# Kernel tuning notes

Measured on AMD Instinct MI355X. Metric: run time of the kernel, lower is better.

The kernel has to match this reference:

```python
import jax, jax.numpy as jnp
import numpy as np

N = 3072
SIGMA = 1.0
NORM_FACTOR = 90.4756
TWOPI = 2.0 * np.pi
NORM_CONST = NORM_FACTOR / TWOPI
A = 1.0 / (SIGMA * 2.0 ** 0.5)
SQRT_PI = np.pi ** 0.5


def setup_inputs() -> dict:
    key = jax.random.key(0)
    ks = jax.random.split(key, 6)
    q = jax.random.normal(ks[0], (N,), dtype=jnp.float32)
    r = jax.random.uniform(ks[1], (N, 3), dtype=jnp.float32) * 30.0  # 30A box
    cell = jnp.zeros((1, 3, 3), dtype=jnp.float32)  # det<1e-6 -> realspace path
    batch = jnp.zeros((N,), dtype=jnp.int32)
    u = jax.random.normal(ks[2], (N, 3), dtype=jnp.float32)
    kappa = jax.random.uniform(ks[3], (N,), dtype=jnp.float32)
    alpha = jax.random.uniform(ks[4], (N,), dtype=jnp.float32)
    return {"q": q, "r": r, "cell": cell, "batch": batch, "u": u, "kappa": kappa, "alpha": alpha}


def _ewald_realspace(q, r, u, kappa, alpha):
    # q:[n], r:[n,3], u:[n,3], kappa:[n], alpha:[n]; single batch, n_q=1 path
    n = q.shape[0]
    eye = jnp.eye(n, dtype=r.dtype)
    off = 1.0 - eye  # mask_off
    r_ij = r[None, :, :] - r[:, None, :]            # [n,n,3], r_j - r_i
    d2 = jnp.sum(r_ij * r_ij, axis=-1)
    rnorm = jnp.sqrt(d2 + eye)                      # diag padded with 1 for grad safety
    rinv = off / rnorm                              # 0 on diagonal
    rinv2 = rinv * rinv
    rinv3 = rinv2 * rinv
    erf = jax.scipy.special.erf(rnorm * A) * off    # 0 on diagonal
    gauss = jnp.exp(-(A * rnorm) ** 2) * off

    # charge-charge
    f_qq = erf * rinv * NORM_CONST
    e_phi = jnp.einsum('i,ij->j', q, f_qq)
    pot = 0.5 * jnp.dot(e_phi, q)

    # dipole kernels
    s1 = erf * rinv3 - (2.0 * A / SQRT_PI) * gauss * rinv2
    s2 = 3.0 * erf * rinv3 - (6.0 * A / SQRT_PI) * gauss * rinv2 - (4.0 * A ** 3 / SQRT_PI) * gauss

    # charge-dipole: f_qu[i,j,c] = s1[i,j]*r_ij[i,j,c]*NORM_CONST (contracted on the fly)
    ur = jnp.einsum('ic,ijc->ij', u, r_ij)          # u_i . r_ij
    e_phi_u = NORM_CONST * jnp.einsum('ij,ij->j', s1, ur)
    e_phi = e_phi + e_phi_u
    pot = pot + jnp.dot(e_phi_u, q)

    # dipole-dipole: f_uu = NORM_CONST*(s2 * rhat rhat^T - s1 * I), contracted without [n,n,3,3]
    rhat = r_ij * rinv[..., None]
    ai = jnp.einsum('ic,ijc->ij', u, rhat)          # u_i . rhat_ij
    bj = jnp.einsum('jc,ijc->ij', u, rhat)          # u_j . rhat_ij
    uu = u @ u.T
    pot = pot - 0.5 * NORM_CONST * (jnp.sum(s2 * ai * bj) - jnp.sum(s1 * uu))

    # induced charges (remove_self_interaction=True: no self terms)
    q_induced = -kappa * e_phi
    pot = pot + 0.5 * jnp.dot(e_phi, q_induced)

    # electric field (alpha is not None -> computed)
    e_field = NORM_CONST * jnp.einsum('i,ij,ijc->jc', q, s1, r_ij)
    E_u = NORM_CONST * (jnp.einsum('ij,ijd->jd', s2 * ai, rhat) - s1.T @ u)
    e_field = e_field + E_u

    # induced dipoles (alpha scalar per node)
    u_induced = e_field * alpha[:, None]
    pot = pot - 0.5 * jnp.sum(e_field * u_induced)

    return pot.reshape(1), q_induced, u_induced


def reference(q, r, cell, batch, u, kappa, alpha):
    # cell is zeros (det < 1e-6) and batch is all-zeros -> single-system realspace branch
    return _ewald_realspace(q, r, u, kappa, alpha)
```

## Files before the change

### kernel.cpp

```cpp
#include <hip/hip_runtime.h>
#include <hip/hip_bf16.h>

#define NATOMS 3072
#define CHUNKS 16
#define WPB 4
#define IPW (NATOMS / (CHUNKS * WPB))

static_assert(IPW * CHUNKS * WPB == NATOMS, "partition must cover all atoms");

constexpr float NCf = (float)(90.4756 / (2.0 * 3.14159265358979323846));
constexpr float Af = 0.70710678118654752f;
constexpr float Cf = 0.79788456080286536f;

__global__ __launch_bounds__(256)
void ewald_pack(const float* __restrict__ q, const float* __restrict__ r,
                const float* __restrict__ u, float4* __restrict__ P,
                float4* __restrict__ U) {
  const int i = blockIdx.x * blockDim.x + threadIdx.x;
  if (i < NATOMS) {
    P[i] = make_float4(r[3 * i + 0], r[3 * i + 1], r[3 * i + 2], q[i]);
    U[i] = make_float4(u[3 * i + 0], u[3 * i + 1], u[3 * i + 2], 0.0f);
  }
}

__global__ __launch_bounds__(256)
void ewald_main(const float4* __restrict__ P, const float4* __restrict__ U,
                float* __restrict__ part) {
  const int lane = threadIdx.x & 63;
  const int w = threadIdx.x >> 6;
  const int j = blockIdx.x * 64 + lane;
  const float4 pj = P[j];

  float acc[8] = {0.f, 0.f, 0.f, 0.f, 0.f, 0.f, 0.f, 0.f};

  const int i0 = (blockIdx.y * WPB + w) * IPW;
#pragma unroll 4
  for (int t = 0; t < IPW; ++t) {
    const int i = i0 + t;
    const float4 pi = P[i];
    const float4 ui = U[i];
    const float dx = pj.x - pi.x;
    const float dy = pj.y - pi.y;
    const float dz = pj.z - pi.z;
    float d2 = dx * dx + dy * dy + dz * dz;
    const bool diag = (i == j);
    if (diag) d2 = 1.0f;
    const float off = diag ? 0.0f : 1.0f;

    const float rinv = __builtin_amdgcn_rsqf(d2);
    const float rinv2 = rinv * rinv;
    const float rinv3 = rinv2 * rinv;
    const float rnorm = d2 * rinv;
    const float x = Af * rnorm;
    const float g0 = __expf(-0.5f * d2);
    const float tt = __builtin_amdgcn_rcpf(fmaf(0.3275911f, x, 1.0f));
    const float poly =
        tt * (0.254829592f +
              tt * (-0.284496736f +
                    tt * (1.421413741f +
                          tt * (-1.453152027f + tt * 1.061405429f))));
    const float erfv = (1.0f - poly * g0) * off;
    const float cg = Cf * (g0 * off);
    const float s1 = erfv * rinv3 - cg * rinv2;
    const float s2 = 3.0f * s1 - cg;

    acc[0] += pi.w * (erfv * rinv);
    const float ur = ui.x * dx + ui.y * dy + ui.z * dz;
    acc[1] += s1 * ur;
    const float qs1 = pi.w * s1;
    acc[2] += qs1 * dx;
    acc[3] += qs1 * dy;
    acc[4] += qs1 * dz;
    const float t2 = s2 * (ur * rinv) * rinv;
    acc[5] += t2 * dx - s1 * ui.x;
    acc[6] += t2 * dy - s1 * ui.y;
    acc[7] += t2 * dz - s1 * ui.z;
  }

  __shared__ float red[(WPB - 1) * 64 * 8];
  if (w > 0) {
    float* dst = &red[((w - 1) * 64 + lane) * 8];
#pragma unroll
    for (int k = 0; k < 8; ++k) dst[k] = acc[k];
  }
  __syncthreads();
  if (w == 0) {
#pragma unroll
    for (int ww = 0; ww < WPB - 1; ++ww) {
      const float* src = &red[(ww * 64 + lane) * 8];
#pragma unroll
      for (int k = 0; k < 8; ++k) acc[k] += src[k];
    }
    float4* dst = (float4*)&part[((size_t)blockIdx.y * NATOMS + j) * 8];
    dst[0] = make_float4(acc[0], acc[1], acc[2], acc[3]);
    dst[1] = make_float4(acc[4], acc[5], acc[6], acc[7]);
  }
}

__global__ __launch_bounds__(256)
void ewald_finalize(const float* __restrict__ part, const float* __restrict__ q,
                    const float* __restrict__ u, const float* __restrict__ kappa,
                    const float* __restrict__ alpha, float* __restrict__ out) {
  const int j = blockIdx.x * blockDim.x + threadIdx.x;

  float s[8] = {0.f, 0.f, 0.f, 0.f, 0.f, 0.f, 0.f, 0.f};
#pragma unroll
  for (int c = 0; c < CHUNKS; ++c) {
    const float4* src = (const float4*)&part[((size_t)c * NATOMS + j) * 8];
    const float4 a = src[0];
    const float4 b = src[1];
    s[0] += a.x; s[1] += a.y; s[2] += a.z; s[3] += a.w;
    s[4] += b.x; s[5] += b.y; s[6] += b.z; s[7] += b.w;
  }

  const float e_phi = NCf * (s[0] + s[1]);
  const float Eux = NCf * s[5];
  const float Euy = NCf * s[6];
  const float Euz = NCf * s[7];
  const float efx = NCf * s[2] + Eux;
  const float efy = NCf * s[3] + Euy;
  const float efz = NCf * s[4] + Euz;

  const float qj = q[j];
  const float kj = kappa[j];
  const float aj = alpha[j];
  const float ujx = u[3 * j + 0];
  const float ujy = u[3 * j + 1];
  const float ujz = u[3 * j + 2];

  out[1 + j] = -kj * e_phi;
  out[1 + NATOMS + 3 * j + 0] = aj * efx;
  out[1 + NATOMS + 3 * j + 1] = aj * efy;
  out[1 + NATOMS + 3 * j + 2] = aj * efz;

  float potj = 0.5f * NCf * s[0] * qj
             + NCf * s[1] * qj
             - 0.5f * (ujx * Eux + ujy * Euy + ujz * Euz)
             - 0.5f * kj * e_phi * e_phi
             - 0.5f * aj * (efx * efx + efy * efy + efz * efz);

#pragma unroll
  for (int m = 32; m >= 1; m >>= 1) potj += __shfl_xor(potj, m, 64);
  __shared__ float lred[4];
  const int lane = threadIdx.x & 63;
  const int wid = threadIdx.x >> 6;
  if (lane == 0) lred[wid] = potj;
  __syncthreads();
  if (threadIdx.x == 0) {
    atomicAdd(out, lred[0] + lred[1] + lred[2] + lred[3]);
  }
}

extern "C" void kernel_launch(void* const* d_in, const int* in_sizes, int n_in,
                              void* d_out, int out_size, void* d_ws,
                              size_t ws_size, hipStream_t stream) {
  const float* q = (const float*)d_in[0];
  const float* r = (const float*)d_in[1];
  const float* u = (const float*)d_in[4];
  const float* kappa = (const float*)d_in[5];
  const float* alpha = (const float*)d_in[6];
  float* out = (float*)d_out;

  float4* P = (float4*)d_ws;
  float4* U = P + NATOMS;
  float* part = (float*)(U + NATOMS);

  hipMemsetAsync(out, 0, sizeof(float), stream);
  ewald_pack<<<dim3((NATOMS + 255) / 256), 256, 0, stream>>>(q, r, u, P, U);
  ewald_main<<<dim3(NATOMS / 64, CHUNKS), 256, 0, stream>>>(P, U, part);
  ewald_finalize<<<dim3(NATOMS / 256), 256, 0, stream>>>(part, q, u, kappa,
                                                         alpha, out);
}
```

Before: 93.73 us.

## Fuse pack into main kernel with LDS staging and drop memset launch

Removes the separate pack kernel and the memset: each block of the main kernel loads its i-chunk of positions, charges and dipoles straight from the raw inputs into shared memory, and block (0,0) zeroes the potential output. CHUNKS doubles to 32, which doubles the grid and the partial buffer that finalize reads. The aim is to cut launch overhead and global-load latency in the inner loop, at the cost of more partial-sum traffic and an extra barrier.

```diff
diff --git a/kernel.cpp b/kernel.cpp
--- a/kernel.cpp
+++ b/kernel.cpp
@@ -2,46 +2,51 @@
 #include <hip/hip_bf16.h>
 
 #define NATOMS 3072
-#define CHUNKS 16
+#define CHUNKS 32
 #define WPB 4
-#define IPW (NATOMS / (CHUNKS * WPB))
+#define IPB (NATOMS / CHUNKS)
+#define IPW (IPB / WPB)
 
-static_assert(IPW * CHUNKS * WPB == NATOMS, "partition must cover all atoms");
+static_assert(IPB * CHUNKS == NATOMS, "i-partition must cover all atoms");
+static_assert(IPW * WPB == IPB, "wave split must cover block chunk");
 
 constexpr float NCf = (float)(90.4756 / (2.0 * 3.14159265358979323846));
 constexpr float Af = 0.70710678118654752f;
 constexpr float Cf = 0.79788456080286536f;
 
 __global__ __launch_bounds__(256)
-void ewald_pack(const float* __restrict__ q, const float* __restrict__ r,
-                const float* __restrict__ u, float4* __restrict__ P,
-                float4* __restrict__ U) {
-  const int i = blockIdx.x * blockDim.x + threadIdx.x;
-  if (i < NATOMS) {
-    P[i] = make_float4(r[3 * i + 0], r[3 * i + 1], r[3 * i + 2], q[i]);
-    U[i] = make_float4(u[3 * i + 0], u[3 * i + 1], u[3 * i + 2], 0.0f);
-  }
-}
-
-__global__ __launch_bounds__(256)
-void ewald_main(const float4* __restrict__ P, const float4* __restrict__ U,
-                float* __restrict__ part) {
+void ewald_main(const float* __restrict__ q, const float* __restrict__ r,
+                const float* __restrict__ u, float* __restrict__ part,
+                float* __restrict__ out) {
   const int lane = threadIdx.x & 63;
   const int w = threadIdx.x >> 6;
   const int j = blockIdx.x * 64 + lane;
-  const float4 pj = P[j];
+
+  if (blockIdx.x == 0 && blockIdx.y == 0 && threadIdx.x == 0) out[0] = 0.0f;
+
+  __shared__ float4 sPU[2 * IPB];
+  const int i0 = blockIdx.y * IPB;
+  for (int t = threadIdx.x; t < IPB; t += 256) {
+    const int i = i0 + t;
+    sPU[2 * t + 0] = make_float4(r[3 * i + 0], r[3 * i + 1], r[3 * i + 2], q[i]);
+    sPU[2 * t + 1] = make_float4(u[3 * i + 0], u[3 * i + 1], u[3 * i + 2], 0.0f);
+  }
+  const float pjx = r[3 * j + 0];
+  const float pjy = r[3 * j + 1];
+  const float pjz = r[3 * j + 2];
+  __syncthreads();
 
   float acc[8] = {0.f, 0.f, 0.f, 0.f, 0.f, 0.f, 0.f, 0.f};
 
-  const int i0 = (blockIdx.y * WPB + w) * IPW;
-#pragma unroll 4
-  for (int t = 0; t < IPW; ++t) {
+  const int t0 = w * IPW;
+#pragma unroll 6
+  for (int t = t0; t < t0 + IPW; ++t) {
+    const float4 pi = sPU[2 * t + 0];
+    const float4 ui = sPU[2 * t + 1];
     const int i = i0 + t;
-    const float4 pi = P[i];
-    const float4 ui = U[i];
-    const float dx = pj.x - pi.x;
-    const float dy = pj.y - pi.y;
-    const float dz = pj.z - pi.z;
+    const float dx = pjx - pi.x;
+    const float dy = pjy - pi.y;
+    const float dz = pjz - pi.z;
     float d2 = dx * dx + dy * dy + dz * dz;
     const bool diag = (i == j);
     if (diag) d2 = 1.0f;
@@ -78,6 +83,7 @@
   }
 
   __shared__ float red[(WPB - 1) * 64 * 8];
+  __syncthreads();
   if (w > 0) {
     float* dst = &red[((w - 1) * 64 + lane) * 8];
 #pragma unroll
@@ -161,13 +167,9 @@
   const float* alpha = (const float*)d_in[6];
   float* out = (float*)d_out;
 
-  float4* P = (float4*)d_ws;
-  float4* U = P + NATOMS;
-  float* part = (float*)(U + NATOMS);
+  float* part = (float*)d_ws;
 
-  hipMemsetAsync(out, 0, sizeof(float), stream);
-  ewald_pack<<<dim3((NATOMS + 255) / 256), 256, 0, stream>>>(q, r, u, P, U);
-  ewald_main<<<dim3(NATOMS / 64, CHUNKS), 256, 0, stream>>>(P, U, part);
+  ewald_main<<<dim3(NATOMS / 64, CHUNKS), 256, 0, stream>>>(q, r, u, part, out);
   ewald_finalize<<<dim3(NATOMS / 256), 256, 0, stream>>>(part, q, u, kappa,
                                                          alpha, out);
 }
```

Measured after the change: 91.46 us. 2.4% less time.
